# Optimization experiments

Hardware: AMD Instinct MI355X
Metric: run time of the kernel (lower is better)

## Reference

```python
import jax, jax.numpy as jnp
import numpy as np

B, S, D, H = 2, 2048, 1024, 16
DK = D // H
THETA = 10000.0


def apply_rope(x, pos, theta):
    # x: [B, H, S, DK], pos: [S]
    dk = x.shape[-1]
    inv_freq = 1.0 / (theta ** (jnp.arange(0, dk, 2, dtype=jnp.float32) / dk))  # [DK/2]
    ang = pos.astype(jnp.float32)[:, None] * inv_freq[None, :]  # [S, DK/2]
    cos, sin = jnp.cos(ang), jnp.sin(ang)
    x1 = x[..., 0::2]  # even dims
    x2 = x[..., 1::2]  # odd dims
    r1 = x1 * cos - x2 * sin
    r2 = x1 * sin + x2 * cos
    # re-interleave pairs back into last dim
    return jnp.stack([r1, r2], axis=-1).reshape(x.shape)


def setup_inputs() -> dict:
    key = jax.random.key(0)
    k1, k2, k3 = jax.random.split(key, 3)
    in_features = jax.random.normal(k1, (B, S, D), dtype=jnp.float32)
    token_positions = jnp.arange(S, dtype=jnp.int32)
    Wqkv = jax.random.normal(k2, (D, 3 * D), dtype=jnp.float32) * 0.02
    Wo = jax.random.normal(k3, (D, D), dtype=jnp.float32) * 0.02
    return {"in_features": in_features, "token_positions": token_positions,
            "Wqkv": Wqkv, "Wo": Wo}


def reference(in_features, token_positions, Wqkv, Wo):
    x = in_features
    qkv = x @ Wqkv  # [B, S, 3D]
    Q, K, V = jnp.split(qkv, 3, axis=-1)

    def to_heads(t):  # [B, S, D] -> [B, H, S, DK]
        return t.reshape(B, S, H, DK).transpose(0, 2, 1, 3)

    Q, K, V = to_heads(Q), to_heads(K), to_heads(V)
    Q = apply_rope(Q, token_positions, THETA)
    K = apply_rope(K, token_positions, THETA)

    scale = 1.0 / jnp.sqrt(jnp.float32(DK))
    scores = jnp.einsum("bhqd,bhkd->bhqk", Q, K) * scale  # [B, H, S, S]
    causal = jnp.tril(jnp.ones((S, S), dtype=bool))
    scores = jnp.where(causal, scores, jnp.finfo(scores.dtype).min)
    attn = jax.nn.softmax(scores, axis=-1)
    out = jnp.einsum("bhqk,bhkd->bhqd", attn, V)  # [B, H, S, DK]
    out = out.transpose(0, 2, 1, 3).reshape(B, S, D)
    return out @ Wo
```

## Files before the change

### kernel.cpp

```cpp
#include <hip/hip_runtime.h>
#include <hip/hip_bf16.h>
#include <math.h>

typedef unsigned short u16;
typedef unsigned int u32;
typedef __attribute__((ext_vector_type(4))) float f32x4;
typedef __attribute__((ext_vector_type(8))) short bf16x8;

#define B_ 2
#define S_ 2048
#define D_ 1024
#define H_ 16
#define DK_ 64

__device__ __forceinline__ float exp2_fast(float x) {
    return __builtin_amdgcn_exp2f(x);
}

__device__ __forceinline__ u16 f2bf(float x) {
    union { __hip_bfloat16 h; u16 u; } v;
    v.h = __float2bfloat16(x);
    return v.u;
}

__device__ __forceinline__ u32 cvt_pk_bf16(float a, float b) {
    u32 r;
    asm("v_cvt_pk_bf16_f32 %0, %1, %2" : "=v"(r) : "v"(a), "v"(b));
    return r;
}

__device__ __forceinline__ void gload_lds16(const u16* g, u16* l) {
    __builtin_amdgcn_global_load_lds(
        (const __attribute__((address_space(1))) unsigned int*)g,
        (__attribute__((address_space(3))) unsigned int*)l, 16, 0, 0);
}

__global__ __launch_bounds__(256) void cast_bf16_kernel(
    const float* __restrict__ in, u16* __restrict__ outp, int n)
{
    const int i = (blockIdx.x * 256 + threadIdx.x) * 8;
    if (i >= n) return;
    float4 a = *(const float4*)(in + i);
    float4 b = *(const float4*)(in + i + 4);
    u32 p0 = (u32)f2bf(a.x) | ((u32)f2bf(a.y) << 16);
    u32 p1 = (u32)f2bf(a.z) | ((u32)f2bf(a.w) << 16);
    u32 p2 = (u32)f2bf(b.x) | ((u32)f2bf(b.y) << 16);
    u32 p3 = (u32)f2bf(b.z) | ((u32)f2bf(b.w) << 16);
    *(uint4*)(outp + i) = make_uint4(p0, p1, p2, p3);
}

__global__ __launch_bounds__(256) void transpose_cast(
    const float* __restrict__ W, u16* __restrict__ WT, int N)
{
    __shared__ float tile[64][65];
    const int k0 = blockIdx.x * 64, n0 = blockIdx.y * 64;
    const int t = threadIdx.x;
    const int r = t >> 4, c4 = (t & 15) * 4;
#pragma unroll
    for (int p = 0; p < 4; ++p) {
        float4 v = *(const float4*)&W[(size_t)(k0 + r + p * 16) * N + n0 + c4];
        tile[r + p * 16][c4 + 0] = v.x;
        tile[r + p * 16][c4 + 1] = v.y;
        tile[r + p * 16][c4 + 2] = v.z;
        tile[r + p * 16][c4 + 3] = v.w;
    }
    __syncthreads();
    const int nl = t >> 2, kc = (t & 3) * 16;
    u16 buf[16];
#pragma unroll
    for (int j = 0; j < 16; ++j) buf[j] = f2bf(tile[kc + j][nl]);
    const size_t idx = (size_t)(n0 + nl) * 1024 + k0 + kc;
    u32 px[8];
#pragma unroll
    for (int j = 0; j < 8; ++j) px[j] = (u32)buf[2 * j] | ((u32)buf[2 * j + 1] << 16);
    *(uint4*)&WT[idx]     = make_uint4(px[0], px[1], px[2], px[3]);
    *(uint4*)&WT[idx + 8] = make_uint4(px[4], px[5], px[6], px[7]);
}

__global__ __launch_bounds__(256) void rope_table_kernel(
    const int* __restrict__ pos, float2* __restrict__ tab)
{
    const int i = blockIdx.x * 256 + threadIdx.x;
    const int s = i >> 5, j = i & 31;
    const float freq = __powf(10000.f, -(float)(2 * j) * (1.f / 64.f));
    const float ang = (float)pos[s] * freq;
    float sn, cs;
    sincosf(ang, &sn, &cs);
    tab[i] = make_float2(cs, sn);
}

__device__ __forceinline__ void gemm_mainloop_128x64(
    const u16* __restrict__ A, const u16* __restrict__ BT, int K,
    int m0, int n0, int tid, int l, int w,
    u16* lA, u16* lB, f32x4 acc[2][4])
{
    const int wr = w >> 1, wc = w & 1, lr = l & 15, lg = l >> 4;
    const int srow = tid >> 3;
    const int cg   = (tid & 7) ^ (srow & 7);
    const u16* gA = A + (size_t)(m0 + srow) * K + cg * 8;
    const u16* gB = BT + (size_t)(n0 + srow) * K + cg * 8;
    const int dst0 = tid * 8;

#define GSTAGE(k0, off)                                              \
    do {                                                             \
        gload_lds16(gA + (k0),          lA + (off) + dst0);          \
        gload_lds16(gA + (k0) + 64 * K, lA + (off) + 4096 + dst0);   \
        gload_lds16(gB + (k0),          lB + (off) + dst0);          \
        gload_lds16(gB + (k0) + 64 * K, lB + (off) + 4096 + dst0);   \
    } while (0)

    GSTAGE(0, 0);

    const int NT = K >> 6;
    for (int t = 0; t < NT; ++t) {
        const int coff = (t & 1) * 8192;
        if (t + 1 < NT) {
            GSTAGE((t + 1) * 64, coff ^ 8192);
            asm volatile("s_waitcnt vmcnt(4)" ::: "memory");
        } else {
            asm volatile("s_waitcnt vmcnt(0)" ::: "memory");
        }
        __builtin_amdgcn_s_barrier();
        __builtin_amdgcn_sched_barrier(0);

        bf16x8 a[2][2], b[4][2];
#pragma unroll
        for (int i = 0; i < 2; ++i) {
            const int row = wr * 32 + i * 16 + lr;
#pragma unroll
            for (int s = 0; s < 2; ++s)
                a[i][s] = *(const bf16x8*)(lA + coff + row * 64 + (((s * 4 + lg) ^ (row & 7)) * 8));
        }
#pragma unroll
        for (int j = 0; j < 4; ++j) {
            const int row = wc * 64 + j * 16 + lr;
#pragma unroll
            for (int s = 0; s < 2; ++s)
                b[j][s] = *(const bf16x8*)(lB + coff + row * 64 + (((s * 4 + lg) ^ (row & 7)) * 8));
        }
#pragma unroll
        for (int s = 0; s < 2; ++s)
#pragma unroll
            for (int i = 0; i < 2; ++i)
#pragma unroll
                for (int j = 0; j < 4; ++j)
                    acc[i][j] = __builtin_amdgcn_mfma_f32_16x16x32_bf16(a[i][s], b[j][s], acc[i][j], 0, 0, 0);

        asm volatile("s_waitcnt lgkmcnt(0)" ::: "memory");
        __builtin_amdgcn_s_barrier();
        __builtin_amdgcn_sched_barrier(0);
    }
#undef GSTAGE
}

__global__ __launch_bounds__(512, 4) void gemm_qkv_rope(
    const u16* __restrict__ A, const u16* __restrict__ BT,
    const float2* __restrict__ tab,
    u16* __restrict__ qo, u16* __restrict__ ko, u16* __restrict__ vto)
{
    __shared__ u16 lA[2 * 128 * 64];
    __shared__ u16 lB[2 * 128 * 64];
    const int tid = threadIdx.x, l = tid & 63, w = tid >> 6;
    const int m0 = blockIdx.x * 128, n0 = blockIdx.y * 128;

    f32x4 acc[2][4] = {};
    gemm_mainloop_128x64(A, BT, 1024, m0, n0, tid, l, w, lA, lB, acc);

    const int wr = w >> 1, wc = w & 1, lr = l & 15, lg = l >> 4;
    const int region = n0 >> 10;

    if (region < 2) {
        u16* dst = (region == 0) ? qo : ko;
        const float qscale = (region == 0) ? (0.125f * 1.44269504088896f) : 1.0f;
#pragma unroll
        for (int j = 0; j < 4; ++j) {
            const int nb = n0 + wc * 64 + j * 16;
            const int h = (nb >> 6) & 15;
            const int c = j * 16 + lr;
#pragma unroll
            for (int i = 0; i < 2; ++i) {
#pragma unroll
                for (int r = 0; r < 4; ++r) {
                    const int m = m0 + wr * 32 + i * 16 + lg * 4 + r;
                    const int bb = m >> 11, s = m & (S_ - 1);
                    const float2 cs = tab[s * 32 + (c >> 1)];
                    const float v = acc[i][j][r];
                    const float vp = __shfl_xor(v, 1);
                    float outv = ((lr & 1) == 0) ? (v * cs.x - vp * cs.y)
                                                 : (v * cs.x + vp * cs.y);
                    outv *= qscale;
                    dst[(((size_t)bb * H_ + h) * S_ + s) * DK_ + c] = f2bf(outv);
                }
            }
        }
    } else {
#pragma unroll
        for (int j = 0; j < 4; ++j) {
            const int nb = n0 + wc * 64 + j * 16;
            const int h = (nb >> 6) & 15;
            const int c = j * 16 + lr;
#pragma unroll
            for (int i = 0; i < 2; ++i) {
#pragma unroll
                for (int r = 0; r < 4; ++r) {
                    const int m = m0 + wr * 32 + i * 16 + lg * 4 + r;
                    const int bb = m >> 11, s = m & (S_ - 1);
                    vto[(((size_t)bb * H_ + h) * DK_ + c) * S_ + s] = f2bf(acc[i][j][r]);
                }
            }
        }
    }
}

__device__ __forceinline__ void stage_tile(
    const u16* __restrict__ Kbh, const u16* __restrict__ Vbh, int kt,
    u16* sKb, u16* sVb, int w, int sr0, int cg)
{
    gload_lds16(Kbh + ((size_t)kt * 64 + sr0) * DK_ + cg * 8,     sKb + w * 1024);
    gload_lds16(Kbh + ((size_t)kt * 64 + sr0 + 8) * DK_ + cg * 8, sKb + w * 1024 + 512);
    gload_lds16(Vbh + (size_t)sr0 * S_ + kt * 64 + cg * 8,        sVb + w * 1024);
    gload_lds16(Vbh + (size_t)(sr0 + 8) * S_ + kt * 64 + cg * 8,  sVb + w * 1024 + 512);
}

__device__ __forceinline__ void attn_stripe(
    int qt, int bh, int w, int l, int lr, int lg,
    const u16* __restrict__ Qg, const u16* __restrict__ Kg,
    const u16* __restrict__ VTg, u16* __restrict__ Og,
    u16 (*sK)[64 * 64], u16 (*sV)[64 * 64])
{
    const int q0 = qt * 64 + w * 16;
    const u16* Kbh = Kg + (size_t)bh * S_ * DK_;
    const u16* Vbh = VTg + (size_t)bh * DK_ * S_;

    const u16* Qp = Qg + ((size_t)bh * S_ + q0) * DK_;
    bf16x8 qa[2];
    qa[0] = *(const bf16x8*)(Qp + lr * DK_ + lg * 8);
    qa[1] = *(const bf16x8*)(Qp + lr * DK_ + 32 + lg * 8);

    const int sr0 = w * 16 + (l >> 3);
    const int cg  = (l & 7) ^ (sr0 & 7);

    f32x4 o[4] = {};
    float mi = -3.0e38f, li = 0.f;

    const int s0 = lr + 32 * (lg & 1);
    const int s1 = s0 + 16;
    const bool hi2 = (lg >= 2);

    stage_tile(Kbh, Vbh, 0, sK[0], sV[0], w, sr0, cg);
    asm volatile("s_waitcnt vmcnt(0)" ::: "memory");
    __syncthreads();

    for (int kt = 0; kt <= qt; ++kt) {
        const int cur = kt & 1;
        if (kt < qt)
            stage_tile(Kbh, Vbh, kt + 1, sK[cur ^ 1], sV[cur ^ 1], w, sr0, cg);

        f32x4 s4[4] = {};
        __builtin_amdgcn_s_setprio(1);
#pragma unroll
        for (int kf = 0; kf < 4; ++kf) {
            const int row = kf * 16 + lr;
#pragma unroll
            for (int ks = 0; ks < 2; ++ks) {
                bf16x8 kb = *(const bf16x8*)(&sK[cur][row * 64 + (((ks * 4 + lg) ^ (row & 7)) * 8)]);
                s4[kf] = __builtin_amdgcn_mfma_f32_16x16x32_bf16(kb, qa[ks], s4[kf], 0, 0, 0);
            }
        }
        __builtin_amdgcn_s_setprio(0);
        if (kt == qt) {
            const int qloc = w * 16 + lr;
#pragma unroll
            for (int kf = 0; kf < 4; ++kf)
#pragma unroll
                for (int r = 0; r < 4; ++r)
                    if (kf * 16 + lg * 4 + r > qloc) s4[kf][r] = -3.0e38f;
        }

        float mx = s4[0][0];
#pragma unroll
        for (int kf = 0; kf < 4; ++kf)
#pragma unroll
            for (int r = 0; r < 4; ++r) mx = fmaxf(mx, s4[kf][r]);
        mx = fmaxf(mx, __shfl_xor(mx, 16));
        mx = fmaxf(mx, __shfl_xor(mx, 32));
        if (mx > mi + 8.0f) {
            const float al = exp2_fast(mi - mx);
            mi = mx;
            li *= al;
#pragma unroll
            for (int jf = 0; jf < 4; ++jf)
#pragma unroll
                for (int r = 0; r < 4; ++r) o[jf][r] *= al;
        }
        float rs = 0.f;
#pragma unroll
        for (int kf = 0; kf < 4; ++kf)
#pragma unroll
            for (int r = 0; r < 4; ++r) {
                const float p = exp2_fast(s4[kf][r] - mi);
                s4[kf][r] = p;
                rs += p;
            }
        rs += __shfl_xor(rs, 16);
        rs += __shfl_xor(rs, 32);
        li += rs;

        u32 pk[4][2];
#pragma unroll
        for (int kf = 0; kf < 4; ++kf) {
            pk[kf][0] = cvt_pk_bf16(s4[kf][0], s4[kf][1]);
            pk[kf][1] = cvt_pk_bf16(s4[kf][2], s4[kf][3]);
        }
        union { u32 wd[4]; bf16x8 v; } pa[2];
#pragma unroll
        for (int ks = 0; ks < 2; ++ks) {
            const u32 lo0 = pk[2 * ks][0],     lo1 = pk[2 * ks][1];
            const u32 hi0 = pk[2 * ks + 1][0], hi1 = pk[2 * ks + 1][1];
            const u32 a0 = __shfl(lo0, s0), b0 = __shfl(hi0, s0);
            const u32 a1 = __shfl(lo1, s0), b1 = __shfl(hi1, s0);
            const u32 a2 = __shfl(lo0, s1), b2 = __shfl(hi0, s1);
            const u32 a3 = __shfl(lo1, s1), b3 = __shfl(hi1, s1);
            pa[ks].wd[0] = hi2 ? b0 : a0;
            pa[ks].wd[1] = hi2 ? b1 : a1;
            pa[ks].wd[2] = hi2 ? b2 : a2;
            pa[ks].wd[3] = hi2 ? b3 : a3;
        }

        __builtin_amdgcn_s_setprio(1);
#pragma unroll
        for (int ks = 0; ks < 2; ++ks) {
#pragma unroll
            for (int jf = 0; jf < 4; ++jf) {
                const int row = jf * 16 + lr;
                bf16x8 vb = *(const bf16x8*)(&sV[cur][row * 64 + (((ks * 4 + lg) ^ (row & 7)) * 8)]);
                o[jf] = __builtin_amdgcn_mfma_f32_16x16x32_bf16(vb, pa[ks].v, o[jf], 0, 0, 0);
            }
        }
        __builtin_amdgcn_s_setprio(0);

        asm volatile("s_waitcnt vmcnt(0)" ::: "memory");
        __syncthreads();
    }

    const float inv = 1.f / li;
    const int b = bh >> 4, h = bh & 15;
    const int srow = q0 + lr;
    u16* orow = Og + ((size_t)b * S_ + srow) * D_ + h * DK_;
#pragma unroll
    for (int jf = 0; jf < 4; ++jf) {
#pragma unroll
        for (int p = 0; p < 2; ++p) {
            const u32 wv = cvt_pk_bf16(o[jf][2 * p] * inv, o[jf][2 * p + 1] * inv);
            *(u32*)(orow + jf * 16 + lg * 4 + 2 * p) = wv;
        }
    }
}

__global__ __launch_bounds__(256) void attn_mfma(
    const u16* __restrict__ Qg, const u16* __restrict__ Kg,
    const u16* __restrict__ VTg, u16* __restrict__ Og)
{
    __shared__ u16 sK[2][64 * 64];
    __shared__ u16 sV[2][64 * 64];
    const int t = threadIdx.x, l = t & 63, w = t >> 6;
    const int lr = l & 15, lg = l >> 4;
    const int bh = blockIdx.x;
    const int pair = blockIdx.y;
    attn_stripe(pair,      bh, w, l, lr, lg, Qg, Kg, VTg, Og, sK, sV);
    attn_stripe(31 - pair, bh, w, l, lr, lg, Qg, Kg, VTg, Og, sK, sV);
}

__global__ __launch_bounds__(512, 4) void gemm_out(
    const u16* __restrict__ A, const u16* __restrict__ BT, float* __restrict__ C)
{
    __shared__ u16 lA[2 * 128 * 64];
    __shared__ u16 lB[2 * 128 * 64];
    const int tid = threadIdx.x, l = tid & 63, w = tid >> 6;
    const int m0 = blockIdx.x * 128, n0 = blockIdx.y * 128;

    f32x4 acc[2][4] = {};
    gemm_mainloop_128x64(A, BT, 1024, m0, n0, tid, l, w, lA, lB, acc);

    const int wr = w >> 1, wc = w & 1, lr = l & 15, lg = l >> 4;
#pragma unroll
    for (int j = 0; j < 4; ++j) {
        const int n = n0 + wc * 64 + j * 16 + lr;
#pragma unroll
        for (int i = 0; i < 2; ++i) {
#pragma unroll
            for (int r = 0; r < 4; ++r) {
                const int m = m0 + wr * 32 + i * 16 + lg * 4 + r;
                C[(size_t)m * D_ + n] = acc[i][j][r];
            }
        }
    }
}

extern "C" void kernel_launch(void* const* d_in, const int* in_sizes, int n_in,
                              void* d_out, int out_size, void* d_ws, size_t ws_size,
                              hipStream_t stream) {
    const float* X    = (const float*)d_in[0];
    const int*   pos  = (const int*)d_in[1];
    const float* Wqkv = (const float*)d_in[2];
    const float* Wo   = (const float*)d_in[3];
    float* out = (float*)d_out;

    char* ws = (char*)d_ws;
    u16*    Xb  = (u16*)(ws);
    u16*    WqT = (u16*)(ws + ((size_t)8  << 20));
    u16*    WoT = (u16*)(ws + ((size_t)14 << 20));
    float2* tab = (float2*)(ws + ((size_t)16 << 20));
    u16*    Qb  = (u16*)(ws + ((size_t)17 << 20));
    u16*    Kb  = (u16*)(ws + ((size_t)25 << 20));
    u16*    VTb = (u16*)(ws + ((size_t)33 << 20));
    u16*    AOb = (u16*)(ws + ((size_t)41 << 20));

    cast_bf16_kernel<<<2048, 256, 0, stream>>>(X, Xb, B_ * S_ * D_);
    transpose_cast<<<dim3(16, 48), 256, 0, stream>>>(Wqkv, WqT, 3 * D_);
    transpose_cast<<<dim3(16, 16), 256, 0, stream>>>(Wo, WoT, D_);
    rope_table_kernel<<<256, 256, 0, stream>>>(pos, tab);

    gemm_qkv_rope<<<dim3(32, 24), 512, 0, stream>>>(Xb, WqT, tab, Qb, Kb, VTb);
    attn_mfma<<<dim3(32, 16), 256, 0, stream>>>(Qb, Kb, VTb, AOb);
    gemm_out<<<dim3(32, 8), 512, 0, stream>>>(AOb, WoT, out);
}
```

Measured before the change: 118.5 us.

## Process 128-row query blocks per workgroup instead of paired 64-row stripes

The attention kernel now gives each workgroup one 128-query block (32 rows per wave, as two 16-row groups) rather than two mirrored 64-row stripes. Each staged K/V tile is reused by twice as many query rows, which halves K/V global loads and syncs per unit of work. The blocks are ordered largest-first so the heaviest work launches early. In exchange it uses more registers for the doubled accumulators, loses the pairing-based load balance, and waves idle on the diagonal tiles where one of their groups is already finished.

```diff
diff --git a/kernel.cpp b/kernel.cpp
--- a/kernel.cpp
+++ b/kernel.cpp
@@ -222,141 +222,6 @@
     gload_lds16(Vbh + (size_t)(sr0 + 8) * S_ + kt * 64 + cg * 8,  sVb + w * 1024 + 512);
 }
 
-__device__ __forceinline__ void attn_stripe(
-    int qt, int bh, int w, int l, int lr, int lg,
-    const u16* __restrict__ Qg, const u16* __restrict__ Kg,
-    const u16* __restrict__ VTg, u16* __restrict__ Og,
-    u16 (*sK)[64 * 64], u16 (*sV)[64 * 64])
-{
-    const int q0 = qt * 64 + w * 16;
-    const u16* Kbh = Kg + (size_t)bh * S_ * DK_;
-    const u16* Vbh = VTg + (size_t)bh * DK_ * S_;
-
-    const u16* Qp = Qg + ((size_t)bh * S_ + q0) * DK_;
-    bf16x8 qa[2];
-    qa[0] = *(const bf16x8*)(Qp + lr * DK_ + lg * 8);
-    qa[1] = *(const bf16x8*)(Qp + lr * DK_ + 32 + lg * 8);
-
-    const int sr0 = w * 16 + (l >> 3);
-    const int cg  = (l & 7) ^ (sr0 & 7);
-
-    f32x4 o[4] = {};
-    float mi = -3.0e38f, li = 0.f;
-
-    const int s0 = lr + 32 * (lg & 1);
-    const int s1 = s0 + 16;
-    const bool hi2 = (lg >= 2);
-
-    stage_tile(Kbh, Vbh, 0, sK[0], sV[0], w, sr0, cg);
-    asm volatile("s_waitcnt vmcnt(0)" ::: "memory");
-    __syncthreads();
-
-    for (int kt = 0; kt <= qt; ++kt) {
-        const int cur = kt & 1;
-        if (kt < qt)
-            stage_tile(Kbh, Vbh, kt + 1, sK[cur ^ 1], sV[cur ^ 1], w, sr0, cg);
-
-        f32x4 s4[4] = {};
-        __builtin_amdgcn_s_setprio(1);
-#pragma unroll
-        for (int kf = 0; kf < 4; ++kf) {
-            const int row = kf * 16 + lr;
-#pragma unroll
-            for (int ks = 0; ks < 2; ++ks) {
-                bf16x8 kb = *(const bf16x8*)(&sK[cur][row * 64 + (((ks * 4 + lg) ^ (row & 7)) * 8)]);
-                s4[kf] = __builtin_amdgcn_mfma_f32_16x16x32_bf16(kb, qa[ks], s4[kf], 0, 0, 0);
-            }
-        }
-        __builtin_amdgcn_s_setprio(0);
-        if (kt == qt) {
-            const int qloc = w * 16 + lr;
-#pragma unroll
-            for (int kf = 0; kf < 4; ++kf)
-#pragma unroll
-                for (int r = 0; r < 4; ++r)
-                    if (kf * 16 + lg * 4 + r > qloc) s4[kf][r] = -3.0e38f;
-        }
-
-        float mx = s4[0][0];
-#pragma unroll
-        for (int kf = 0; kf < 4; ++kf)
-#pragma unroll
-            for (int r = 0; r < 4; ++r) mx = fmaxf(mx, s4[kf][r]);
-        mx = fmaxf(mx, __shfl_xor(mx, 16));
-        mx = fmaxf(mx, __shfl_xor(mx, 32));
-        if (mx > mi + 8.0f) {
-            const float al = exp2_fast(mi - mx);
-            mi = mx;
-            li *= al;
-#pragma unroll
-            for (int jf = 0; jf < 4; ++jf)
-#pragma unroll
-                for (int r = 0; r < 4; ++r) o[jf][r] *= al;
-        }
-        float rs = 0.f;
-#pragma unroll
-        for (int kf = 0; kf < 4; ++kf)
-#pragma unroll
-            for (int r = 0; r < 4; ++r) {
-                const float p = exp2_fast(s4[kf][r] - mi);
-                s4[kf][r] = p;
-                rs += p;
-            }
-        rs += __shfl_xor(rs, 16);
-        rs += __shfl_xor(rs, 32);
-        li += rs;
-
-        u32 pk[4][2];
-#pragma unroll
-        for (int kf = 0; kf < 4; ++kf) {
-            pk[kf][0] = cvt_pk_bf16(s4[kf][0], s4[kf][1]);
-            pk[kf][1] = cvt_pk_bf16(s4[kf][2], s4[kf][3]);
-        }
-        union { u32 wd[4]; bf16x8 v; } pa[2];
-#pragma unroll
-        for (int ks = 0; ks < 2; ++ks) {
-            const u32 lo0 = pk[2 * ks][0],     lo1 = pk[2 * ks][1];
-            const u32 hi0 = pk[2 * ks + 1][0], hi1 = pk[2 * ks + 1][1];
-            const u32 a0 = __shfl(lo0, s0), b0 = __shfl(hi0, s0);
-            const u32 a1 = __shfl(lo1, s0), b1 = __shfl(hi1, s0);
-            const u32 a2 = __shfl(lo0, s1), b2 = __shfl(hi0, s1);
-            const u32 a3 = __shfl(lo1, s1), b3 = __shfl(hi1, s1);
-            pa[ks].wd[0] = hi2 ? b0 : a0;
-            pa[ks].wd[1] = hi2 ? b1 : a1;
-            pa[ks].wd[2] = hi2 ? b2 : a2;
-            pa[ks].wd[3] = hi2 ? b3 : a3;
-        }
-
-        __builtin_amdgcn_s_setprio(1);
-#pragma unroll
-        for (int ks = 0; ks < 2; ++ks) {
-#pragma unroll
-            for (int jf = 0; jf < 4; ++jf) {
-                const int row = jf * 16 + lr;
-                bf16x8 vb = *(const bf16x8*)(&sV[cur][row * 64 + (((ks * 4 + lg) ^ (row & 7)) * 8)]);
-                o[jf] = __builtin_amdgcn_mfma_f32_16x16x32_bf16(vb, pa[ks].v, o[jf], 0, 0, 0);
-            }
-        }
-        __builtin_amdgcn_s_setprio(0);
-
-        asm volatile("s_waitcnt vmcnt(0)" ::: "memory");
-        __syncthreads();
-    }
-
-    const float inv = 1.f / li;
-    const int b = bh >> 4, h = bh & 15;
-    const int srow = q0 + lr;
-    u16* orow = Og + ((size_t)b * S_ + srow) * D_ + h * DK_;
-#pragma unroll
-    for (int jf = 0; jf < 4; ++jf) {
-#pragma unroll
-        for (int p = 0; p < 2; ++p) {
-            const u32 wv = cvt_pk_bf16(o[jf][2 * p] * inv, o[jf][2 * p + 1] * inv);
-            *(u32*)(orow + jf * 16 + lg * 4 + 2 * p) = wv;
-        }
-    }
-}
-
 __global__ __launch_bounds__(256) void attn_mfma(
     const u16* __restrict__ Qg, const u16* __restrict__ Kg,
     const u16* __restrict__ VTg, u16* __restrict__ Og)
@@ -366,9 +231,152 @@
     const int t = threadIdx.x, l = t & 63, w = t >> 6;
     const int lr = l & 15, lg = l >> 4;
     const int bh = blockIdx.x;
-    const int pair = blockIdx.y;
-    attn_stripe(pair,      bh, w, l, lr, lg, Qg, Kg, VTg, Og, sK, sV);
-    attn_stripe(31 - pair, bh, w, l, lr, lg, Qg, Kg, VTg, Og, sK, sV);
+    const int qb = 15 - blockIdx.y;
+    const int q0 = qb * 128;
+    const int NT = 2 * qb + 2;
+
+    const u16* Kbh = Kg + (size_t)bh * S_ * DK_;
+    const u16* Vbh = VTg + (size_t)bh * DK_ * S_;
+    const u16* Qp = Qg + ((size_t)bh * S_ + q0 + w * 32) * DK_;
+
+    bf16x8 qa[2][2];
+#pragma unroll
+    for (int g = 0; g < 2; ++g) {
+        qa[g][0] = *(const bf16x8*)(Qp + (g * 16 + lr) * DK_ + lg * 8);
+        qa[g][1] = *(const bf16x8*)(Qp + (g * 16 + lr) * DK_ + 32 + lg * 8);
+    }
+
+    const int sr0 = w * 16 + (l >> 3);
+    const int cg  = (l & 7) ^ (sr0 & 7);
+
+    f32x4 o[2][4] = {};
+    float mi[2] = { -3.0e38f, -3.0e38f }, li[2] = { 0.f, 0.f };
+    const int dt0 = (q0 + w * 32) >> 6;
+    const int dt1 = (q0 + w * 32 + 16) >> 6;
+    const int ql0 = ((w * 32) & 63) + lr;
+    const int ql1 = ((w * 32 + 16) & 63) + lr;
+
+    const int s0 = lr + 32 * (lg & 1);
+    const int s1 = s0 + 16;
+    const bool hi2 = (lg >= 2);
+
+    stage_tile(Kbh, Vbh, 0, sK[0], sV[0], w, sr0, cg);
+    asm volatile("s_waitcnt vmcnt(0)" ::: "memory");
+    __syncthreads();
+
+    for (int kt = 0; kt < NT; ++kt) {
+        const int cur = kt & 1;
+        if (kt + 1 < NT)
+            stage_tile(Kbh, Vbh, kt + 1, sK[cur ^ 1], sV[cur ^ 1], w, sr0, cg);
+
+#pragma unroll
+        for (int g = 0; g < 2; ++g) {
+            const int dtg = g ? dt1 : dt0;
+            if (kt > dtg) continue;
+            const int qlg = g ? ql1 : ql0;
+
+            f32x4 s4[4] = {};
+            __builtin_amdgcn_s_setprio(1);
+#pragma unroll
+            for (int kf = 0; kf < 4; ++kf) {
+                const int row = kf * 16 + lr;
+#pragma unroll
+                for (int ks = 0; ks < 2; ++ks) {
+                    bf16x8 kb = *(const bf16x8*)(&sK[cur][row * 64 + (((ks * 4 + lg) ^ (row & 7)) * 8)]);
+                    s4[kf] = __builtin_amdgcn_mfma_f32_16x16x32_bf16(kb, qa[g][ks], s4[kf], 0, 0, 0);
+                }
+            }
+            __builtin_amdgcn_s_setprio(0);
+            if (kt == dtg) {
+#pragma unroll
+                for (int kf = 0; kf < 4; ++kf)
+#pragma unroll
+                    for (int r = 0; r < 4; ++r)
+                        if (kf * 16 + lg * 4 + r > qlg) s4[kf][r] = -3.0e38f;
+            }
+
+            float mx = s4[0][0];
+#pragma unroll
+            for (int kf = 0; kf < 4; ++kf)
+#pragma unroll
+                for (int r = 0; r < 4; ++r) mx = fmaxf(mx, s4[kf][r]);
+            mx = fmaxf(mx, __shfl_xor(mx, 16));
+            mx = fmaxf(mx, __shfl_xor(mx, 32));
+            if (mx > mi[g] + 8.0f) {
+                const float al = exp2_fast(mi[g] - mx);
+                mi[g] = mx;
+                li[g] *= al;
+#pragma unroll
+                for (int jf = 0; jf < 4; ++jf)
+#pragma unroll
+                    for (int r = 0; r < 4; ++r) o[g][jf][r] *= al;
+            }
+            float rs = 0.f;
+#pragma unroll
+            for (int kf = 0; kf < 4; ++kf)
+#pragma unroll
+                for (int r = 0; r < 4; ++r) {
+                    const float p = exp2_fast(s4[kf][r] - mi[g]);
+                    s4[kf][r] = p;
+                    rs += p;
+                }
+            rs += __shfl_xor(rs, 16);
+            rs += __shfl_xor(rs, 32);
+            li[g] += rs;
+
+            u32 pk[4][2];
+#pragma unroll
+            for (int kf = 0; kf < 4; ++kf) {
+                pk[kf][0] = cvt_pk_bf16(s4[kf][0], s4[kf][1]);
+                pk[kf][1] = cvt_pk_bf16(s4[kf][2], s4[kf][3]);
+            }
+            union { u32 wd[4]; bf16x8 v; } pa[2];
+#pragma unroll
+            for (int ks = 0; ks < 2; ++ks) {
+                const u32 lo0 = pk[2 * ks][0],     lo1 = pk[2 * ks][1];
+                const u32 hi0 = pk[2 * ks + 1][0], hi1 = pk[2 * ks + 1][1];
+                const u32 a0 = __shfl(lo0, s0), b0 = __shfl(hi0, s0);
+                const u32 a1 = __shfl(lo1, s0), b1 = __shfl(hi1, s0);
+                const u32 a2 = __shfl(lo0, s1), b2 = __shfl(hi0, s1);
+                const u32 a3 = __shfl(lo1, s1), b3 = __shfl(hi1, s1);
+                pa[ks].wd[0] = hi2 ? b0 : a0;
+                pa[ks].wd[1] = hi2 ? b1 : a1;
+                pa[ks].wd[2] = hi2 ? b2 : a2;
+                pa[ks].wd[3] = hi2 ? b3 : a3;
+            }
+
+            __builtin_amdgcn_s_setprio(1);
+#pragma unroll
+            for (int ks = 0; ks < 2; ++ks) {
+#pragma unroll
+                for (int jf = 0; jf < 4; ++jf) {
+                    const int row = jf * 16 + lr;
+                    bf16x8 vb = *(const bf16x8*)(&sV[cur][row * 64 + (((ks * 4 + lg) ^ (row & 7)) * 8)]);
+                    o[g][jf] = __builtin_amdgcn_mfma_f32_16x16x32_bf16(vb, pa[ks].v, o[g][jf], 0, 0, 0);
+                }
+            }
+            __builtin_amdgcn_s_setprio(0);
+        }
+
+        asm volatile("s_waitcnt vmcnt(0)" ::: "memory");
+        __syncthreads();
+    }
+
+    const int b = bh >> 4, h = bh & 15;
+#pragma unroll
+    for (int g = 0; g < 2; ++g) {
+        const float inv = 1.f / li[g];
+        const int srow = q0 + w * 32 + g * 16 + lr;
+        u16* orow = Og + ((size_t)b * S_ + srow) * D_ + h * DK_;
+#pragma unroll
+        for (int jf = 0; jf < 4; ++jf) {
+#pragma unroll
+            for (int p = 0; p < 2; ++p) {
+                const u32 wv = cvt_pk_bf16(o[g][jf][2 * p] * inv, o[g][jf][2 * p + 1] * inv);
+                *(u32*)(orow + jf * 16 + lg * 4 + 2 * p) = wv;
+            }
+        }
+    }
 }
 
 __global__ __launch_bounds__(512, 4) void gemm_out(
```

Result: slower. 142.4 us (+20.2%).
